# Kernel tuning notes

Measured on AMD Instinct MI355X. Metric: run time of the kernel, lower is better.

Reference implementation:

```python
import jax, jax.numpy as jnp
import numpy as np

NUM_TOURS = 200   # fixed segment count (original: tour_index.max()+1)
EPS = 1e-5        # torch InstanceNorm1d default eps


def setup_inputs() -> dict:
    key = jax.random.key(0)
    ks = jax.random.split(key, 9)
    B, P, D = 64, 2000, 128
    embeddings = jax.random.normal(ks[0], (B, P + 1, D), jnp.float32)
    tour_index = jax.random.randint(ks[1], (B, P), 0, NUM_TOURS, dtype=jnp.int32)
    # tour_combiner: Linear(2D -> D); feedforward: Linear(D -> D); stored as (in, out)
    W1 = jax.random.normal(ks[2], (2 * D, D), jnp.float32) / np.sqrt(2 * D)
    b1 = jax.random.normal(ks[3], (D,), jnp.float32) * 0.01
    W2 = jax.random.normal(ks[4], (D, D), jnp.float32) / np.sqrt(D)
    b2 = jax.random.normal(ks[5], (D,), jnp.float32) * 0.01
    # InstanceNorm1d affine params (per channel)
    gamma = 1.0 + 0.1 * jax.random.normal(ks[6], (D,), jnp.float32)
    beta = 0.1 * jax.random.normal(ks[7], (D,), jnp.float32)
    return {
        "batch_size": B, "num_customers": P,
        "tour_index": tour_index, "embeddings": embeddings,
        "W1": W1, "b1": b1, "W2": W2, "b2": b2,
        "gamma": gamma, "beta": beta,
    }


def reference(batch_size, num_customers, tour_index, embeddings, W1, b1, W2, b2, gamma, beta):
    B, P = batch_size, num_customers
    D = embeddings.shape[-1]
    cust = embeddings[:, 1:]                                  # (B, P, D)
    # tour-level segment sum (scatter_add over tour ids, per batch)
    flat_idx = (tour_index + jnp.arange(B, dtype=tour_index.dtype)[:, None] * NUM_TOURS).reshape(-1)
    tour_emb = jax.ops.segment_sum(cust.reshape(B * P, D), flat_idx,
                                   num_segments=B * NUM_TOURS).reshape(B, NUM_TOURS, D)
    # gather tour embedding back to each customer
    cust_tour = jnp.take_along_axis(tour_emb, tour_index[:, :, None], axis=1)  # (B, P, D)
    # concat -> linear -> relu -> linear
    combined = jnp.concatenate([cust, cust_tour], axis=-1)    # (B, P, 2D)
    h = jax.nn.relu(combined @ W1 + b1)
    h = h @ W2 + b2
    # residual + instance norm over the customer axis, per channel
    added = cust + h
    mean = jnp.mean(added, axis=1, keepdims=True)
    var = jnp.var(added, axis=1, keepdims=True)
    normed = (added - mean) * jax.lax.rsqrt(var + EPS) * gamma + beta
    return jnp.concatenate([embeddings[:, :1], normed], axis=1)
```

## Files before the change

### kernel.cpp

```cpp
#include <hip/hip_runtime.h>
#include <stdint.h>

typedef unsigned short u16;
typedef __attribute__((ext_vector_type(8))) short short8;
typedef __attribute__((ext_vector_type(4))) float floatx4;

constexpr int B_ = 64, P_ = 2000, D_ = 128, T_ = 200;

__device__ __forceinline__ u16 f2bf(float f) {
  union { float f; uint32_t u; } v; v.f = f;
  return (u16)((v.u + 0x7fffu + ((v.u >> 16) & 1u)) >> 16);
}

__global__ __launch_bounds__(256) void k_pre(
    const int* __restrict__ tidx, int* __restrict__ list,
    int* __restrict__ goff, int* __restrict__ gcnt,
    const float* __restrict__ W1, const float* __restrict__ W2,
    u16* __restrict__ w1f, u16* __restrict__ w2f, float* __restrict__ ssum) {
  __shared__ int tix[P_];
  __shared__ int cnt[256], scan[256], cur[256];
  const int bid = blockIdx.x, tid = threadIdx.x;

  if (bid >= 64) {
    if (bid < 128) {
      ssum[(bid - 64) * 256 + tid] = 0.f;
      return;
    }
    int t = (bid - 128) * 256 + tid;
    if (t >= 6144) return;
    const float* W = (t < 4096) ? W1 : W2;
    u16* dst = (t < 4096) ? w1f : w2f;
    int fid = (t < 4096) ? t : t - 4096;
    int lane = fid & 63;
    int nt = (fid >> 6) & 7;
    int ks = fid >> 9;
    int quad = lane >> 4, c = lane & 15;
    int k0 = ks * 32 + quad * 8;
#pragma unroll
    for (int j = 0; j < 8; ++j)
      dst[(size_t)fid * 8 + j] = f2bf(W[(k0 + j) * D_ + nt * 16 + c]);
    return;
  }

  const int b = bid;
  cnt[tid] = 0;
  for (int i = tid; i < P_; i += 256) tix[i] = tidx[b * P_ + i];
  __syncthreads();
  for (int i = tid; i < P_; i += 256) atomicAdd(&cnt[tix[i]], 1);
  __syncthreads();
  scan[tid] = cnt[tid];
  __syncthreads();
  for (int s = 1; s < 256; s <<= 1) {
    int v = (tid >= s) ? scan[tid - s] : 0;
    __syncthreads();
    scan[tid] += v;
    __syncthreads();
  }
  int excl = scan[tid] - cnt[tid];
  if (tid < T_) {
    goff[b * T_ + tid] = excl;
    gcnt[b * T_ + tid] = cnt[tid];
  }
  cur[tid] = excl;
  __syncthreads();
  for (int i = tid; i < P_; i += 256) {
    int slot = atomicAdd(&cur[tix[i]], 1);
    list[b * P_ + slot] = i;
  }
}

__global__ __launch_bounds__(256) void k_gather(const float* __restrict__ emb,
                                                const int* __restrict__ list,
                                                const int* __restrict__ goff,
                                                const int* __restrict__ gcnt,
                                                u16* __restrict__ tourb) {
  const int tid = threadIdx.x;
  const int lane = tid & 63, wv = tid >> 6;
  const int seg = blockIdx.x * 4 + wv;
  const int b = seg / T_;
  const int off = goff[seg], cn = gcnt[seg];
  const int* lstb = list + b * P_;
  const float* eb = emb + ((size_t)(b * 2001 + 1)) * D_ + lane * 2;
  float sx = 0.f, sy = 0.f;
  for (int i = 0; i < cn; i += 8) {
    int pr[8];
#pragma unroll
    for (int j = 0; j < 8; ++j)
      if (i + j < cn) pr[j] = lstb[off + i + j];
    float2 v[8];
#pragma unroll
    for (int j = 0; j < 8; ++j)
      if (i + j < cn) v[j] = *(const float2*)(eb + (size_t)pr[j] * D_);
#pragma unroll
    for (int j = 0; j < 8; ++j)
      if (i + j < cn) { sx += v[j].x; sy += v[j].y; }
  }
  uint32_t pk = (uint32_t)f2bf(sx) | ((uint32_t)f2bf(sy) << 16);
  ((uint32_t*)(tourb + (size_t)seg * D_))[lane] = pk;
}

__global__ __launch_bounds__(256) void k_mlp(
    const int* __restrict__ tidx, const float* __restrict__ emb,
    const u16* __restrict__ tourb,
    const u16* __restrict__ w1f, const u16* __restrict__ w2f,
    const float* __restrict__ b1, const float* __restrict__ b2,
    float* __restrict__ ssum, float* __restrict__ ssq,
    float* __restrict__ out) {
  __shared__ u16 hbuf[128 * 136];
  __shared__ float red[2][2][128];
  const int tid = threadIdx.x;
  const int w = tid >> 6, lane = tid & 63, quad = lane >> 4, c = lane & 15;
  const int base = blockIdx.x * 128;
  const int r0 = w * 32;

  for (int i = tid; i < 512; i += 256) ((float*)red)[i] = 0.f;

  const int blo = base / P_;
  const int bhi = (base + 127) / P_;
  const bool straddle = (blo != bhi);
  const int bsplit = bhi * P_;

  const float* arow[2];
  const u16* trow[2];
#pragma unroll
  for (int mt = 0; mt < 2; ++mt) {
    int m = base + r0 + mt * 16 + c;
    int b = m / P_, p = m - b * P_;
    arow[mt] = emb + ((size_t)(b * 2001 + 1 + p)) * D_;
    int t = tidx[m];
    trow[mt] = tourb + ((size_t)(b * T_ + t)) * D_;
  }
  float bias1[8], bias2[8];
#pragma unroll
  for (int nt = 0; nt < 8; ++nt) {
    bias1[nt] = b1[nt * 16 + c];
    bias2[nt] = b2[nt * 16 + c];
  }

  floatx4 acc[2][8];
#pragma unroll
  for (int mt = 0; mt < 2; ++mt)
#pragma unroll
    for (int nt = 0; nt < 8; ++nt) acc[mt][nt] = (floatx4)0.f;

#pragma unroll
  for (int ks = 0; ks < 8; ++ks) {
    short8 a[2];
#pragma unroll
    for (int mt = 0; mt < 2; ++mt) {
      if (ks < 4) {
        const float* src = arow[mt] + ks * 32 + quad * 8;
        floatx4 x0 = *(const floatx4*)src;
        floatx4 x1 = *(const floatx4*)(src + 4);
#pragma unroll
        for (int j = 0; j < 4; ++j) {
          a[mt][j]     = (short)f2bf(x0[j]);
          a[mt][4 + j] = (short)f2bf(x1[j]);
        }
      } else {
        a[mt] = *(const short8*)(trow[mt] + (ks - 4) * 32 + quad * 8);
      }
    }
#pragma unroll
    for (int nt = 0; nt < 8; ++nt) {
      short8 bf = *(const short8*)(w1f + ((size_t)((ks * 8 + nt) * 64 + lane)) * 8);
      acc[0][nt] = __builtin_amdgcn_mfma_f32_16x16x32_bf16(a[0], bf, acc[0][nt], 0, 0, 0);
      acc[1][nt] = __builtin_amdgcn_mfma_f32_16x16x32_bf16(a[1], bf, acc[1][nt], 0, 0, 0);
    }
  }

#pragma unroll
  for (int mt = 0; mt < 2; ++mt)
#pragma unroll
    for (int nt = 0; nt < 8; ++nt)
#pragma unroll
      for (int r = 0; r < 4; ++r) {
        int row = r0 + mt * 16 + quad * 4 + r;
        float v = acc[mt][nt][r] + bias1[nt];
        hbuf[row * 136 + nt * 16 + c] = f2bf(v > 0.f ? v : 0.f);
      }
  __syncthreads();

  floatx4 acc2[2][8];
#pragma unroll
  for (int mt = 0; mt < 2; ++mt)
#pragma unroll
    for (int nt = 0; nt < 8; ++nt) acc2[mt][nt] = (floatx4)0.f;

#pragma unroll
  for (int ks = 0; ks < 4; ++ks) {
    short8 a[2];
#pragma unroll
    for (int mt = 0; mt < 2; ++mt)
      a[mt] = *(const short8*)(&hbuf[(r0 + mt * 16 + c) * 136 + ks * 32 + quad * 8]);
#pragma unroll
    for (int nt = 0; nt < 8; ++nt) {
      short8 bf = *(const short8*)(w2f + ((size_t)((ks * 8 + nt) * 64 + lane)) * 8);
      acc2[0][nt] = __builtin_amdgcn_mfma_f32_16x16x32_bf16(a[0], bf, acc2[0][nt], 0, 0, 0);
      acc2[1][nt] = __builtin_amdgcn_mfma_f32_16x16x32_bf16(a[1], bf, acc2[1][nt], 0, 0, 0);
    }
  }

  float s[8], q[8];
#pragma unroll
  for (int nt = 0; nt < 8; ++nt) { s[nt] = 0.f; q[nt] = 0.f; }
#pragma unroll
  for (int mt = 0; mt < 2; ++mt)
#pragma unroll
    for (int nt = 0; nt < 8; ++nt)
#pragma unroll
      for (int r = 0; r < 4; ++r) {
        int row = r0 + mt * 16 + quad * 4 + r;
        int m = base + row;
        int b = m / P_, p = m - b * P_;
        size_t gaddr = ((size_t)(b * 2001 + 1 + p)) * D_ + nt * 16 + c;
        float v = emb[gaddr] + (acc2[mt][nt][r] + bias2[nt]);
        out[gaddr] = v;
        if (!straddle || m < bsplit) {
          s[nt] += v; q[nt] += v * v;
        } else {
          atomicAdd(&red[1][0][nt * 16 + c], v);
          atomicAdd(&red[1][1][nt * 16 + c], v * v);
        }
      }
#pragma unroll
  for (int nt = 0; nt < 8; ++nt) {
    s[nt] += __shfl_xor(s[nt], 16);
    s[nt] += __shfl_xor(s[nt], 32);
    q[nt] += __shfl_xor(q[nt], 16);
    q[nt] += __shfl_xor(q[nt], 32);
  }
  if (quad == 0) {
#pragma unroll
    for (int nt = 0; nt < 8; ++nt) {
      atomicAdd(&red[0][0][nt * 16 + c], s[nt]);
      atomicAdd(&red[0][1][nt * 16 + c], q[nt]);
    }
  }
  __syncthreads();
  if (tid < 128) {
    atomicAdd(&ssum[blo * D_ + tid], red[0][0][tid]);
    if (straddle) atomicAdd(&ssum[bhi * D_ + tid], red[1][0][tid]);
  } else {
    int col = tid - 128;
    atomicAdd(&ssq[blo * D_ + col], red[0][1][col]);
    if (straddle) atomicAdd(&ssq[bhi * D_ + col], red[1][1][col]);
  }
}

__global__ __launch_bounds__(256) void k_out(
    const float* __restrict__ emb,
    const float* __restrict__ ssum, const float* __restrict__ ssq,
    const float* __restrict__ gamma, const float* __restrict__ beta,
    float* __restrict__ out) {
  size_t i = ((size_t)blockIdx.x * 256 + threadIdx.x) * 8;
  int row = (int)(i >> 7), col = (int)(i & 127);
  int b = row / 2001, r = row - b * 2001;
  if (r == 0) {
    *(floatx4*)(out + i)     = *(const floatx4*)(emb + i);
    *(floatx4*)(out + i + 4) = *(const floatx4*)(emb + i + 4);
  } else {
    floatx4 a0 = *(const floatx4*)(out + i);
    floatx4 a1 = *(const floatx4*)(out + i + 4);
    int cc = b * D_ + col;
    floatx4 su0 = *(const floatx4*)(ssum + cc);
    floatx4 su1 = *(const floatx4*)(ssum + cc + 4);
    floatx4 sq0 = *(const floatx4*)(ssq + cc);
    floatx4 sq1 = *(const floatx4*)(ssq + cc + 4);
    floatx4 g0  = *(const floatx4*)(gamma + col);
    floatx4 g1  = *(const floatx4*)(gamma + col + 4);
    floatx4 be0 = *(const floatx4*)(beta + col);
    floatx4 be1 = *(const floatx4*)(beta + col + 4);
    constexpr float invP = 1.f / P_;
#pragma unroll
    for (int j = 0; j < 4; ++j) {
      float mean = su0[j] * invP;
      float var  = sq0[j] * invP - mean * mean;
      float sc   = rsqrtf(var + 1e-5f) * g0[j];
      a0[j] = a0[j] * sc + (be0[j] - mean * sc);
      float mean1 = su1[j] * invP;
      float var1  = sq1[j] * invP - mean1 * mean1;
      float sc1   = rsqrtf(var1 + 1e-5f) * g1[j];
      a1[j] = a1[j] * sc1 + (be1[j] - mean1 * sc1);
    }
    *(floatx4*)(out + i)     = a0;
    *(floatx4*)(out + i + 4) = a1;
  }
}

extern "C" void kernel_launch(void* const* d_in, const int* in_sizes, int n_in,
                              void* d_out, int out_size, void* d_ws, size_t ws_size,
                              hipStream_t stream) {
  const int*   tour_index = (const int*)d_in[2];
  const float* emb   = (const float*)d_in[3];
  const float* W1    = (const float*)d_in[4];
  const float* b1    = (const float*)d_in[5];
  const float* W2    = (const float*)d_in[6];
  const float* b2    = (const float*)d_in[7];
  const float* gamma = (const float*)d_in[8];
  const float* beta  = (const float*)d_in[9];
  float* out = (float*)d_out;
  char* ws = (char*)d_ws;

  u16*   w1f   = (u16*)(ws);
  u16*   w2f   = (u16*)(ws + 65536);
  float* ssum  = (float*)(ws + 98304);
  float* ssq   = ssum + B_ * D_;
  u16*   tourb = (u16*)(ws + 229376);
  int*   list  = (int*)(ws + 3506176);
  int*   goff  = (int*)(ws + 4018176);
  int*   gcnt  = (int*)(ws + 4069376);

  hipLaunchKernelGGL(k_pre,    dim3(152),  dim3(256), 0, stream,
                     tour_index, list, goff, gcnt, W1, W2, w1f, w2f, ssum);
  hipLaunchKernelGGL(k_gather, dim3(3200), dim3(256), 0, stream, emb, list, goff, gcnt, tourb);
  hipLaunchKernelGGL(k_mlp,    dim3(1000), dim3(256), 0, stream, tour_index, emb, tourb,
                     w1f, w2f, b1, b2, ssum, ssq, out);
  hipLaunchKernelGGL(k_out,    dim3(8004), dim3(256), 0, stream, emb, ssum, ssq, gamma, beta, out);
}
```

Measured before the change: 242.6 us.

## Halve k_mlp row tile to 64 rows per block and raise occupancy

Each wave in k_mlp now handles one 16-row M tile instead of two, so a block covers 64 rows and the grid doubles to 2000 blocks. The shared h buffer shrinks and launch_bounds asks for 5 blocks per CU, which cuts accumulator register pressure and allows more waves in flight to hide global load latency. The cost is that each W1/W2 fragment loaded from global memory now feeds only one MFMA instead of two. It also means twice as many blocks issue atomics to the global stats.

```diff
diff --git a/kernel.cpp b/kernel.cpp
--- a/kernel.cpp
+++ b/kernel.cpp
@@ -99,37 +99,32 @@
   ((uint32_t*)(tourb + (size_t)seg * D_))[lane] = pk;
 }
 
-__global__ __launch_bounds__(256) void k_mlp(
+__global__ __launch_bounds__(256, 5) void k_mlp(
     const int* __restrict__ tidx, const float* __restrict__ emb,
     const u16* __restrict__ tourb,
     const u16* __restrict__ w1f, const u16* __restrict__ w2f,
     const float* __restrict__ b1, const float* __restrict__ b2,
     float* __restrict__ ssum, float* __restrict__ ssq,
     float* __restrict__ out) {
-  __shared__ u16 hbuf[128 * 136];
+  __shared__ u16 hbuf[64 * 136];
   __shared__ float red[2][2][128];
   const int tid = threadIdx.x;
   const int w = tid >> 6, lane = tid & 63, quad = lane >> 4, c = lane & 15;
-  const int base = blockIdx.x * 128;
-  const int r0 = w * 32;
+  const int base = blockIdx.x * 64;
+  const int r0 = w * 16;
 
   for (int i = tid; i < 512; i += 256) ((float*)red)[i] = 0.f;
 
   const int blo = base / P_;
-  const int bhi = (base + 127) / P_;
+  const int bhi = (base + 63) / P_;
   const bool straddle = (blo != bhi);
   const int bsplit = bhi * P_;
 
-  const float* arow[2];
-  const u16* trow[2];
-#pragma unroll
-  for (int mt = 0; mt < 2; ++mt) {
-    int m = base + r0 + mt * 16 + c;
-    int b = m / P_, p = m - b * P_;
-    arow[mt] = emb + ((size_t)(b * 2001 + 1 + p)) * D_;
-    int t = tidx[m];
-    trow[mt] = tourb + ((size_t)(b * T_ + t)) * D_;
-  }
+  const int m0 = base + r0 + c;
+  const int ab = m0 / P_, ap = m0 - ab * P_;
+  const float* arow = emb + ((size_t)(ab * 2001 + 1 + ap)) * D_;
+  const u16* trow = tourb + ((size_t)(ab * T_ + tidx[m0])) * D_;
+
   float bias1[8], bias2[8];
 #pragma unroll
   for (int nt = 0; nt < 8; ++nt) {
@@ -137,67 +132,53 @@
     bias2[nt] = b2[nt * 16 + c];
   }
 
-  floatx4 acc[2][8];
-#pragma unroll
-  for (int mt = 0; mt < 2; ++mt)
-#pragma unroll
-    for (int nt = 0; nt < 8; ++nt) acc[mt][nt] = (floatx4)0.f;
+  floatx4 acc[8];
+#pragma unroll
+  for (int nt = 0; nt < 8; ++nt) acc[nt] = (floatx4)0.f;
 
 #pragma unroll
   for (int ks = 0; ks < 8; ++ks) {
-    short8 a[2];
-#pragma unroll
-    for (int mt = 0; mt < 2; ++mt) {
-      if (ks < 4) {
-        const float* src = arow[mt] + ks * 32 + quad * 8;
-        floatx4 x0 = *(const floatx4*)src;
-        floatx4 x1 = *(const floatx4*)(src + 4);
-#pragma unroll
-        for (int j = 0; j < 4; ++j) {
-          a[mt][j]     = (short)f2bf(x0[j]);
-          a[mt][4 + j] = (short)f2bf(x1[j]);
-        }
-      } else {
-        a[mt] = *(const short8*)(trow[mt] + (ks - 4) * 32 + quad * 8);
+    short8 a;
+    if (ks < 4) {
+      const float* src = arow + ks * 32 + quad * 8;
+      floatx4 x0 = *(const floatx4*)src;
+      floatx4 x1 = *(const floatx4*)(src + 4);
+#pragma unroll
+      for (int j = 0; j < 4; ++j) {
+        a[j]     = (short)f2bf(x0[j]);
+        a[4 + j] = (short)f2bf(x1[j]);
       }
+    } else {
+      a = *(const short8*)(trow + (ks - 4) * 32 + quad * 8);
     }
 #pragma unroll
     for (int nt = 0; nt < 8; ++nt) {
       short8 bf = *(const short8*)(w1f + ((size_t)((ks * 8 + nt) * 64 + lane)) * 8);
-      acc[0][nt] = __builtin_amdgcn_mfma_f32_16x16x32_bf16(a[0], bf, acc[0][nt], 0, 0, 0);
-      acc[1][nt] = __builtin_amdgcn_mfma_f32_16x16x32_bf16(a[1], bf, acc[1][nt], 0, 0, 0);
-    }
-  }
-
-#pragma unroll
-  for (int mt = 0; mt < 2; ++mt)
-#pragma unroll
-    for (int nt = 0; nt < 8; ++nt)
-#pragma unroll
-      for (int r = 0; r < 4; ++r) {
-        int row = r0 + mt * 16 + quad * 4 + r;
-        float v = acc[mt][nt][r] + bias1[nt];
-        hbuf[row * 136 + nt * 16 + c] = f2bf(v > 0.f ? v : 0.f);
-      }
-  __syncthreads();
-
-  floatx4 acc2[2][8];
-#pragma unroll
-  for (int mt = 0; mt < 2; ++mt)
-#pragma unroll
-    for (int nt = 0; nt < 8; ++nt) acc2[mt][nt] = (floatx4)0.f;
+      acc[nt] = __builtin_amdgcn_mfma_f32_16x16x32_bf16(a, bf, acc[nt], 0, 0, 0);
+    }
+  }
+
+#pragma unroll
+  for (int nt = 0; nt < 8; ++nt)
+#pragma unroll
+    for (int r = 0; r < 4; ++r) {
+      int row = r0 + quad * 4 + r;
+      float v = acc[nt][r] + bias1[nt];
+      hbuf[row * 136 + nt * 16 + c] = f2bf(v > 0.f ? v : 0.f);
+    }
+  __syncthreads();
+
+  floatx4 acc2[8];
+#pragma unroll
+  for (int nt = 0; nt < 8; ++nt) acc2[nt] = (floatx4)0.f;
 
 #pragma unroll
   for (int ks = 0; ks < 4; ++ks) {
-    short8 a[2];
-#pragma unroll
-    for (int mt = 0; mt < 2; ++mt)
-      a[mt] = *(const short8*)(&hbuf[(r0 + mt * 16 + c) * 136 + ks * 32 + quad * 8]);
+    short8 a = *(const short8*)(&hbuf[(r0 + c) * 136 + ks * 32 + quad * 8]);
 #pragma unroll
     for (int nt = 0; nt < 8; ++nt) {
       short8 bf = *(const short8*)(w2f + ((size_t)((ks * 8 + nt) * 64 + lane)) * 8);
-      acc2[0][nt] = __builtin_amdgcn_mfma_f32_16x16x32_bf16(a[0], bf, acc2[0][nt], 0, 0, 0);
-      acc2[1][nt] = __builtin_amdgcn_mfma_f32_16x16x32_bf16(a[1], bf, acc2[1][nt], 0, 0, 0);
+      acc2[nt] = __builtin_amdgcn_mfma_f32_16x16x32_bf16(a, bf, acc2[nt], 0, 0, 0);
     }
   }
 
@@ -205,24 +186,22 @@
 #pragma unroll
   for (int nt = 0; nt < 8; ++nt) { s[nt] = 0.f; q[nt] = 0.f; }
 #pragma unroll
-  for (int mt = 0; mt < 2; ++mt)
-#pragma unroll
-    for (int nt = 0; nt < 8; ++nt)
-#pragma unroll
-      for (int r = 0; r < 4; ++r) {
-        int row = r0 + mt * 16 + quad * 4 + r;
-        int m = base + row;
-        int b = m / P_, p = m - b * P_;
-        size_t gaddr = ((size_t)(b * 2001 + 1 + p)) * D_ + nt * 16 + c;
-        float v = emb[gaddr] + (acc2[mt][nt][r] + bias2[nt]);
-        out[gaddr] = v;
-        if (!straddle || m < bsplit) {
-          s[nt] += v; q[nt] += v * v;
-        } else {
-          atomicAdd(&red[1][0][nt * 16 + c], v);
-          atomicAdd(&red[1][1][nt * 16 + c], v * v);
-        }
+  for (int nt = 0; nt < 8; ++nt)
+#pragma unroll
+    for (int r = 0; r < 4; ++r) {
+      int row = r0 + quad * 4 + r;
+      int m = base + row;
+      int b = m / P_, p = m - b * P_;
+      size_t gaddr = ((size_t)(b * 2001 + 1 + p)) * D_ + nt * 16 + c;
+      float v = emb[gaddr] + (acc2[nt][r] + bias2[nt]);
+      out[gaddr] = v;
+      if (!straddle || m < bsplit) {
+        s[nt] += v; q[nt] += v * v;
+      } else {
+        atomicAdd(&red[1][0][nt * 16 + c], v);
+        atomicAdd(&red[1][1][nt * 16 + c], v * v);
       }
+    }
 #pragma unroll
   for (int nt = 0; nt < 8; ++nt) {
     s[nt] += __shfl_xor(s[nt], 16);
@@ -314,7 +293,7 @@
   hipLaunchKernelGGL(k_pre,    dim3(152),  dim3(256), 0, stream,
                      tour_index, list, goff, gcnt, W1, W2, w1f, w2f, ssum);
   hipLaunchKernelGGL(k_gather, dim3(3200), dim3(256), 0, stream, emb, list, goff, gcnt, tourb);
-  hipLaunchKernelGGL(k_mlp,    dim3(1000), dim3(256), 0, stream, tour_index, emb, tourb,
+  hipLaunchKernelGGL(k_mlp,    dim3(2000), dim3(256), 0, stream, tour_index, emb, tourb,
                      w1f, w2f, b1, b2, ssum, ssq, out);
   hipLaunchKernelGGL(k_out,    dim3(8004), dim3(256), 0, stream, emb, ssum, ssq, gamma, beta, out);
 }
```

Measured after the change: 223.0 us. 1.09x faster.
